# Optimization experiments

Hardware: AMD Instinct MI355X
Metric: run time of the kernel (lower is better)

Reference implementation:

```python
import jax, jax.numpy as jnp
import numpy as np

GROUPS = 8
N_HEADS = 8
EPS = 1e-5


def setup_inputs() -> dict:
    key = jax.random.key(0)
    ks = jax.random.split(key, 3)
    B, C, H, W = 8, 512, 32, 32
    x = jax.random.normal(ks[0], (B, C, H, W), dtype=jnp.float32)
    # Conv2d(C, 3C, 1) weight squeezed to [3C, C]; kaiming-ish scale
    qkv_w = jax.random.normal(ks[1], (3 * C, C), dtype=jnp.float32) * (1.0 / np.sqrt(C))
    proj_w = jax.random.normal(ks[2], (C, C), dtype=jnp.float32) * (1.0 / np.sqrt(C))
    return {
        "x": x,
        "norm_gamma": jnp.ones((C,), jnp.float32),
        "norm_beta": jnp.zeros((C,), jnp.float32),
        "qkv_w": qkv_w,
        "qkv_b": jnp.zeros((3 * C,), jnp.float32),
        "proj_w": proj_w,
        "proj_b": jnp.zeros((C,), jnp.float32),
    }


def reference(x, norm_gamma, norm_beta, qkv_w, qkv_b, proj_w, proj_b):
    B, C, H, W = x.shape
    nh = N_HEADS
    hd = C // nh
    scale = hd ** (-0.5)
    S = H * W

    # GroupNorm(8, C): normalize over (C/G, H, W) within each group
    xg = x.reshape(B, GROUPS, -1)
    mean = xg.mean(axis=-1, keepdims=True)
    var = xg.var(axis=-1, keepdims=True)
    xn = ((xg - mean) * jax.lax.rsqrt(var + EPS)).reshape(B, C, H, W)
    xn = xn * norm_gamma[None, :, None, None] + norm_beta[None, :, None, None]

    # 1x1 conv QKV == per-pixel matmul
    qkv = jnp.einsum('oc,bchw->bohw', qkv_w, xn) + qkv_b[None, :, None, None]
    qkv = qkv.reshape(B, 3, nh, hd, S)
    q, k, v = qkv[:, 0], qkv[:, 1], qkv[:, 2]  # each (B, nh, hd, S)

    # attn[b,h,s,t] = sum_d q[b,h,d,s] k[b,h,d,t] * scale
    attn = jax.nn.softmax(jnp.einsum('bhds,bhdt->bhst', q, k) * scale, axis=-1)
    out = jnp.einsum('bhst,bhdt->bhds', attn, v).reshape(B, C, H, W)

    # 1x1 conv projection + residual
    return x + jnp.einsum('oc,bchw->bohw', proj_w, out) + proj_b[None, :, None, None]
```

## Files before the change

### kernel.cpp

```cpp
#include <hip/hip_runtime.h>
#include <hip/hip_bf16.h>

typedef __attribute__((ext_vector_type(4))) float  f32x4;
typedef __attribute__((ext_vector_type(8))) _Float16 f16x8;
typedef __attribute__((ext_vector_type(4))) _Float16 f16x4;
typedef __attribute__((ext_vector_type(4))) float  float4v;
typedef __attribute__((ext_vector_type(4))) unsigned int uint4v;

#define BATCH   8
#define CDIM    512
#define SLEN    1024
#define NHEADS  8
#define HDIM    64
#define QSCALE  0.1803368801111f
#define FIXED_M 8.0f


__device__ __forceinline__ f32x4 mfma16x16x16f16(f16x4 a, f16x4 b, f32x4 c){
#if __has_builtin(__builtin_amdgcn_mfma_f32_16x16x16f16)
    return __builtin_amdgcn_mfma_f32_16x16x16f16(a, b, c, 0, 0, 0);
#else
    asm volatile("v_mfma_f32_16x16x16_f16 %0, %1, %2, %0"
                 : "+v"(c) : "v"(a), "v"(b));
    return c;
#endif
}

__device__ __forceinline__ float fast_exp2(float x){
    float r;
    asm("v_exp_f32 %0, %1" : "=v"(r) : "v"(x));
    return r;
}

__device__ __forceinline__ void stage16(const void* g, void* l, int lane){
#if __has_builtin(__builtin_amdgcn_global_load_lds)
    __builtin_amdgcn_global_load_lds((const __attribute__((address_space(1))) void*)g,
                                     (__attribute__((address_space(3))) void*)l, 16, 0, 0);
#else
    *(f16x8*)((char*)l + lane * 16) = *(const f16x8*)g;
#endif
}


__global__ __launch_bounds__(256) void prep(
    const float4v* __restrict__ qkvw, f16x4* __restrict__ wq,
    const float4v* __restrict__ projw, f16x4* __restrict__ pw,
    const float* __restrict__ x, float* __restrict__ part)
{
    __shared__ float s1[256], s2[256];
    if (blockIdx.x < 1024){
        int i = blockIdx.x * 256 + threadIdx.x;
        if (i < 196608){
            float4v v = qkvw[i];
            wq[i] = (f16x4){ (_Float16)v[0], (_Float16)v[1], (_Float16)v[2], (_Float16)v[3] };
        } else {
            int j = i - 196608;
            float4v v = projw[j];
            pw[j] = (f16x4){ (_Float16)v[0], (_Float16)v[1], (_Float16)v[2], (_Float16)v[3] };
        }
        return;
    }
    int bid = blockIdx.x - 1024;
    int bg = bid >> 3, pc = bid & 7;
    const float4v* xp = (const float4v*)(x + (size_t)bg * 65536 + (size_t)pc * 8192);
    float sum = 0.f, sq = 0.f;
    for (int i = threadIdx.x; i < 2048; i += 256){
        float4v v = xp[i];
        sum += (v[0] + v[1]) + (v[2] + v[3]);
        sq  += (v[0]*v[0] + v[1]*v[1]) + (v[2]*v[2] + v[3]*v[3]);
    }
    s1[threadIdx.x] = sum; s2[threadIdx.x] = sq;
    __syncthreads();
    for (int o = 128; o > 0; o >>= 1){
        if (threadIdx.x < o){ s1[threadIdx.x] += s1[threadIdx.x + o];
                              s2[threadIdx.x] += s2[threadIdx.x + o]; }
        __syncthreads();
    }
    if (threadIdx.x == 0){
        part[bid * 2 + 0] = s1[0];
        part[bid * 2 + 1] = s2[0];
    }
}


__global__ __launch_bounds__(256) void gn_apply(
    const float* __restrict__ x, const float* __restrict__ part,
    const float* __restrict__ gamma, const float* __restrict__ beta,
    _Float16* __restrict__ xnT)
{
    int b = blockIdx.z, g = blockIdx.y, s0 = blockIdx.x * 64;
    int bg = b * 8 + g, c0 = g * 64;

    float sum = 0.f, sq = 0.f;
#pragma unroll
    for (int p = 0; p < 8; p++){
        sum += part[bg * 16 + p * 2 + 0];
        sq  += part[bg * 16 + p * 2 + 1];
    }
    float mean = sum * (1.f / 65536.f);
    float var  = sq  * (1.f / 65536.f) - mean * mean;
    float inv  = rsqrtf(var + 1e-5f);

    __shared__ _Float16 tile[64 * 66];

    int tx = threadIdx.x & 15, ty = threadIdx.x >> 4;
#pragma unroll
    for (int j = 0; j < 4; j++){
        int c = ty + 16 * j;
        float ga = gamma[c0 + c] * inv;
        float be = beta[c0 + c] - mean * ga;
        float4v v = *(const float4v*)(x + ((size_t)(b * CDIM + c0 + c)) * SLEN + s0 + tx * 4);
#pragma unroll
        for (int i = 0; i < 4; i++)
            tile[(tx * 4 + i) * 66 + c] = (_Float16)(v[i] * ga + be);
    }
    __syncthreads();

    int s = threadIdx.x >> 2, cq = (threadIdx.x & 3) * 16;
    const unsigned int* lsrc = (const unsigned int*)((const unsigned short*)tile + s * 66 + cq);
    uint4v lo = { lsrc[0], lsrc[1], lsrc[2], lsrc[3] };
    uint4v hi = { lsrc[4], lsrc[5], lsrc[6], lsrc[7] };
    unsigned int* dst = (unsigned int*)(xnT + ((size_t)b * SLEN + s0 + s) * CDIM + c0 + cq);
    *(uint4v*)dst       = lo;
    *(uint4v*)(dst + 4) = hi;
}


#define GEMM_CORE(APTR, BPTR)                                                   \
    __shared__ __align__(16) char smem[34816];                                  \
    int tid = threadIdx.x;                                                      \
    int wid = tid >> 6, lane = tid & 63;                                        \
    int w0 = wid >> 1, w1 = wid & 1;                                            \
    int lr = lane & 15, lg = lane >> 4;                                         \
    int slotg = ((lane & 3) ^ ((lane >> 3) & 3)) * 16;                          \
    int srow = lane >> 2;                                                       \
    const char* agp = (const char*)(APTR) +                                     \
        ((size_t)(bo + wid * 32 + srow) * CDIM) * 2 + slotg;                    \
    const char* bgp = (const char*)(BPTR) +                                     \
        ((size_t)(sgbase + wid * 32 + srow) * CDIM) * 2 + slotg;                \
    char* lA = smem + wid * 2048;                                               \
    char* lB = smem + 8192 + wid * 2048;                                        \
    f32x4 acc[4][4];                                                            \
    _Pragma("unroll") for (int i = 0; i < 4; i++)                               \
    _Pragma("unroll") for (int j = 0; j < 4; j++)                               \
        acc[i][j] = (f32x4){0.f, 0.f, 0.f, 0.f};                                \
    _Pragma("unroll") for (int j = 0; j < 2; j++){                              \
        stage16(agp + j * 16384, lA + j * 1024, lane);                          \
        stage16(bgp + j * 16384, lB + j * 1024, lane);                          \
    }                                                                           \
    __syncthreads();                                                            \
    int xt = ((lr >> 1) & 3) << 4;                                              \
    for (int it = 0; it < 16; ++it){                                            \
        int cur = (it & 1) * 16384;                                             \
        if (it + 1 < 16){                                                       \
            int nxt = 16384 - cur, ko = (it + 1) * 64;                          \
            _Pragma("unroll") for (int j = 0; j < 2; j++){                      \
                stage16(agp + j * 16384 + ko, lA + nxt + j * 1024, lane);       \
                stage16(bgp + j * 16384 + ko, lB + nxt + j * 1024, lane);       \
            }                                                                   \
        }                                                                       \
        const char* Ac = smem + cur + (w0 * 64 + lr) * 64;                      \
        const char* Bc = smem + cur + 8192 + (w1 * 64 + lr) * 64;               \
        f16x8 af[4], bfr[4];                                                    \
        _Pragma("unroll") for (int t = 0; t < 4; t++){                          \
            af[t]  = *(const f16x8*)(Ac + t * 1024 + ((lg * 16) ^ xt));         \
            bfr[t] = *(const f16x8*)(Bc + t * 1024 + ((lg * 16) ^ xt));         \
        }                                                                       \
        _Pragma("unroll") for (int i = 0; i < 4; i++)                           \
        _Pragma("unroll") for (int j = 0; j < 4; j++)                           \
            acc[i][j] = __builtin_amdgcn_mfma_f32_16x16x32_f16(af[i], bfr[j],   \
                                                               acc[i][j], 0, 0, 0); \
        __syncthreads();                                                        \
    }


__global__ __launch_bounds__(256) void qkv_gemm(
    const _Float16* __restrict__ wq, const _Float16* __restrict__ xnT,
    const float* __restrict__ qkvb,
    _Float16* __restrict__ qT, _Float16* __restrict__ kT, _Float16* __restrict__ vv)
{
    int b  = blockIdx.z;
    int bo = blockIdx.y * 128;
    size_t sgbase = (size_t)b * SLEN + blockIdx.x * 128;

    GEMM_CORE(wq, xnT)

    int obase = bo + w0 * 64, sbase = blockIdx.x * 128 + w1 * 64;
    int p = obase >> 9;
    int h = (obase >> 6) & 7;
    size_t bh = (size_t)b * NHEADS + h;

    if (p == 2){
#pragma unroll
        for (int i = 0; i < 4; i++){
            int d0 = i * 16 + lg * 4;
            float4v bias = *(const float4v*)(qkvb + obase + d0);
#pragma unroll
            for (int j = 0; j < 4; j++){
                int s = sbase + j * 16 + lr;
                _Float16* vp2 = vv + (bh * HDIM) * SLEN + s;
                vp2[(size_t)(d0 + 0) * SLEN] = (_Float16)(acc[i][j][0] + bias[0]);
                vp2[(size_t)(d0 + 1) * SLEN] = (_Float16)(acc[i][j][1] + bias[1]);
                vp2[(size_t)(d0 + 2) * SLEN] = (_Float16)(acc[i][j][2] + bias[2]);
                vp2[(size_t)(d0 + 3) * SLEN] = (_Float16)(acc[i][j][3] + bias[3]);
            }
        }
    } else {
        float sc = (p == 0) ? QSCALE : 1.f;
        char* wreg = smem + wid * 8192;
#pragma unroll
        for (int i = 0; i < 4; i++){
            int d0 = i * 16 + lg * 4;
            float4v bias = *(const float4v*)(qkvb + obase + d0);
            int slotbase = (2 * i + (lg >> 1)) * 16;
            int inoff = (lg & 1) * 8;
#pragma unroll
            for (int j = 0; j < 4; j++){
                int s_loc = j * 16 + lr;
                f16x4 pk = { (_Float16)((acc[i][j][0] + bias[0]) * sc),
                             (_Float16)((acc[i][j][1] + bias[1]) * sc),
                             (_Float16)((acc[i][j][2] + bias[2]) * sc),
                             (_Float16)((acc[i][j][3] + bias[3]) * sc) };
                *(f16x4*)(wreg + s_loc * 128 + (slotbase ^ ((s_loc & 7) << 4)) + inoff) = pk;
            }
        }
        _Float16* dst = (p == 0 ? qT : kT) + (bh * SLEN + sbase) * HDIM;
#pragma unroll
        for (int m = 0; m < 8; m++){
            int s_loc = m * 8 + (lane >> 3);
            f16x8 row = *(const f16x8*)(wreg + s_loc * 128 + (((lane & 7) ^ (s_loc & 7)) << 4));
            *(f16x8*)(dst + (size_t)s_loc * HDIM + (lane & 7) * 8) = row;
        }
    }
}


__global__ __launch_bounds__(256) void proj_gemm(
    const _Float16* __restrict__ pw, const _Float16* __restrict__ outT,
    const float* __restrict__ pb, const float* __restrict__ x,
    float* __restrict__ y)
{
    int b  = blockIdx.z;
    int bo = blockIdx.y * 128;
    size_t sgbase = (size_t)b * SLEN + blockIdx.x * 128;

    GEMM_CORE(pw, outT)

    int obase = bo + w0 * 64, sbase = blockIdx.x * 128 + w1 * 64;
    float* wreg = (float*)(smem + wid * 8704);

#pragma unroll
    for (int half = 0; half < 2; half++){
        asm volatile("" ::: "memory");
#pragma unroll
        for (int jj = 0; jj < 2; jj++){
            int j = half * 2 + jj;
            int srow2 = jj * 16 + lr;
#pragma unroll
            for (int i = 0; i < 4; i++){
                int c0 = i * 16 + lg * 4;
                float4v bias = *(const float4v*)(pb + obase + c0);
                float4v v = { acc[i][j][0] + bias[0], acc[i][j][1] + bias[1],
                              acc[i][j][2] + bias[2], acc[i][j][3] + bias[3] };
                *(float4v*)(wreg + srow2 * 68 + c0) = v;
            }
        }
        asm volatile("" ::: "memory");
        int cl = lane >> 3, sq = (lane & 7) * 4;
#pragma unroll
        for (int g = 0; g < 8; g++){
            int c = cl + 8 * g;
            float r0 = wreg[(sq + 0) * 68 + c];
            float r1 = wreg[(sq + 1) * 68 + c];
            float r2 = wreg[(sq + 2) * 68 + c];
            float r3 = wreg[(sq + 3) * 68 + c];
            size_t idx = ((size_t)b * CDIM + obase + c) * SLEN + sbase + half * 32 + sq;
            float4v xr = *(const float4v*)(x + idx);
            float4v o = { r0 + xr[0], r1 + xr[1], r2 + xr[2], r3 + xr[3] };
            *(float4v*)(y + idx) = o;
        }
    }
}


#define ATTN_CHUNK(c)                                                           \
    {                                                                           \
        const char* kbuf = smem + ((c) & 3) * 16384;                            \
        const char* vbuf = kbuf + 8192;                                         \
        f16x8 kf[4][2];                                                         \
        _Pragma("unroll") for (int i = 0; i < 4; i++){                          \
            const char* kr = kbuf + (16 * i + lr) * 128;                        \
            kf[i][0] = *(const f16x8*)(kr + ((lg * 16) ^ r7));                  \
            kf[i][1] = *(const f16x8*)(kr + ((64 + lg * 16) ^ r7));             \
        }                                                                       \
        f16x4 vf[4][4];                                                         \
        _Pragma("unroll") for (int i = 0; i < 4; i++)                           \
        _Pragma("unroll") for (int dt = 0; dt < 4; dt++)                        \
            vf[i][dt] = *(const f16x4*)(vbuf + (dt * 16 + lr) * 128             \
                                        + ((32 * i + 8 * lg) ^ r7));            \
        _Pragma("unroll") for (int sj = 0; sj < 2; sj++){                       \
            f32x4 st[4];                                                        \
            _Pragma("unroll") for (int i = 0; i < 4; i++){                      \
                f32x4 z = (f32x4){-FIXED_M, -FIXED_M, -FIXED_M, -FIXED_M};      \
                z = __builtin_amdgcn_mfma_f32_16x16x32_f16(kf[i][0], qf[sj][0], z, 0, 0, 0); \
                z = __builtin_amdgcn_mfma_f32_16x16x32_f16(kf[i][1], qf[sj][1], z, 0, 0, 0); \
                st[i] = z;                                                      \
            }                                                                   \
            f16x4 pb[4];                                                        \
            _Pragma("unroll") for (int i = 0; i < 4; i++){                      \
                float p0 = fast_exp2(st[i][0]);                                 \
                float p1 = fast_exp2(st[i][1]);                                 \
                float p2 = fast_exp2(st[i][2]);                                 \
                float p3 = fast_exp2(st[i][3]);                                 \
                pb[i] = (f16x4){ (_Float16)p0, (_Float16)p1,                    \
                                 (_Float16)p2, (_Float16)p3 };                  \
            }                                                                   \
            _Pragma("unroll") for (int i = 0; i < 4; i++)                       \
                osum[sj] = mfma16x16x16f16(ones, pb[i], osum[sj]);              \
            _Pragma("unroll") for (int dt = 0; dt < 4; dt++){                   \
                f32x4 o = oac[dt][sj];                                          \
                _Pragma("unroll") for (int i = 0; i < 4; i++)                   \
                    o = mfma16x16x16f16(vf[i][dt], pb[i], o);                   \
                oac[dt][sj] = o;                                                \
            }                                                                   \
        }                                                                       \
    }

__global__ __launch_bounds__(256) void attn_kernel(
    const _Float16* __restrict__ qT, const _Float16* __restrict__ kT,
    const _Float16* __restrict__ vv, _Float16* __restrict__ outT)
{
    __shared__ __align__(16) char smem[65536];

    int id = blockIdx.x;
    int h = id & 7, rr = id >> 3;
    int sx = rr & 7, b = rr >> 3;
    size_t bh = (size_t)b * NHEADS + h;
    int tid = threadIdx.x;
    int wid = tid >> 6, lane = tid & 63;
    int lr = lane & 15, lg = lane >> 4;
    int sbase = sx * 128 + wid * 32;
    int phase = sx << 1;

    const _Float16* qp = qT + bh * SLEN * HDIM;
    const _Float16* kp = kT + bh * SLEN * HDIM;
    const _Float16* vp = vv + bh * HDIM * SLEN;

    int r8 = lane >> 3;
    int srow = wid * 16 + r8;
    int scol = ((lane & 7) * 16) ^ ((srow & 7) << 4);
    const char* kg = (const char*)kp + (size_t)srow * 128  + scol;
    const char* vg = (const char*)vp + (size_t)srow * 2048 + scol;
    char* kd = smem + wid * 2048;
    char* vd = smem + 8192 + wid * 2048;

    f16x8 qf[2][2];
#pragma unroll
    for (int sj = 0; sj < 2; sj++)
#pragma unroll
        for (int kk = 0; kk < 2; kk++)
            qf[sj][kk] = *(const f16x8*)(qp + (size_t)(sbase + sj * 16 + lr) * HDIM + kk * 32 + lg * 8);

    f32x4 oac[4][2], osum[2];
#pragma unroll
    for (int dt = 0; dt < 4; dt++){
        oac[dt][0] = (f32x4){0.f, 0.f, 0.f, 0.f};
        oac[dt][1] = (f32x4){0.f, 0.f, 0.f, 0.f};
    }
    osum[0] = (f32x4){0.f, 0.f, 0.f, 0.f};
    osum[1] = (f32x4){0.f, 0.f, 0.f, 0.f};
    const f16x4 ones = { (_Float16)1.f, (_Float16)1.f, (_Float16)1.f, (_Float16)1.f };

#pragma unroll
    for (int c = 0; c < 2; c++){
        int pc = (c + phase) & 15;
        stage16(kg + (size_t)pc * 8192,         kd + c * 16384,        lane);
        stage16(kg + (size_t)pc * 8192 + 1024,  kd + c * 16384 + 1024, lane);
        stage16(vg + (size_t)pc * 128,          vd + c * 16384,        lane);
        stage16(vg + (size_t)pc * 128 + 16384,  vd + c * 16384 + 1024, lane);
    }
    __syncthreads();

    int r7 = (lr & 7) << 4;

    for (int cc0 = 0; cc0 < 16; cc0 += 2){
        if (cc0 + 2 < 16){
#pragma unroll
            for (int u = 2; u < 4; u++){
                int lc = cc0 + u, pc = (lc + phase) & 15, bb = (lc & 3) * 16384;
                stage16(kg + (size_t)pc * 8192,         kd + bb,        lane);
                stage16(kg + (size_t)pc * 8192 + 1024,  kd + bb + 1024, lane);
                stage16(vg + (size_t)pc * 128,          vd + bb,        lane);
                stage16(vg + (size_t)pc * 128 + 16384,  vd + bb + 1024, lane);
            }
        }
        ATTN_CHUNK(cc0)
        ATTN_CHUNK(cc0 + 1)
        __syncthreads();
    }

#pragma unroll
    for (int sj = 0; sj < 2; sj++){
        float inv = 1.f / osum[sj][0];
        int s = sbase + sj * 16 + lr;
#pragma unroll
        for (int dt = 0; dt < 4; dt++){
            f16x4 ob = { (_Float16)(oac[dt][sj][0] * inv), (_Float16)(oac[dt][sj][1] * inv),
                         (_Float16)(oac[dt][sj][2] * inv), (_Float16)(oac[dt][sj][3] * inv) };
            *(f16x4*)(outT + ((size_t)b * SLEN + s) * CDIM + h * HDIM + dt * 16 + lg * 4) = ob;
        }
    }
}


extern "C" void kernel_launch(void* const* d_in, const int* in_sizes, int n_in,
                              void* d_out, int out_size, void* d_ws, size_t ws_size,
                              hipStream_t stream)
{
    const float* x     = (const float*)d_in[0];
    const float* gamma = (const float*)d_in[1];
    const float* beta  = (const float*)d_in[2];
    const float* qkvw  = (const float*)d_in[3];
    const float* qkvb  = (const float*)d_in[4];
    const float* projw = (const float*)d_in[5];
    const float* projb = (const float*)d_in[6];
    float* out = (float*)d_out;

    char* ws = (char*)d_ws;
    _Float16* wq_bf = (_Float16*)(ws);
    _Float16* pw_bf = (_Float16*)(ws + 1572864);
    _Float16* xnT   = (_Float16*)(ws + 2097152);
    _Float16* qT    = (_Float16*)(ws + 2097152 + 8388608);
    _Float16* kT    = (_Float16*)(ws + 2097152 + 16777216);
    _Float16* vv    = (_Float16*)(ws + 2097152 + 25165824);
    _Float16* outT  = (_Float16*)(ws + 2097152 + 33554432);
    float*    part  = (float*)(ws + 2097152 + 33554432);

    prep<<<1536, 256, 0, stream>>>((const float4v*)qkvw, (f16x4*)wq_bf,
                                   (const float4v*)projw, (f16x4*)pw_bf, x, part);
    gn_apply<<<dim3(16, 8, 8), 256, 0, stream>>>(x, part, gamma, beta, xnT);
    qkv_gemm<<<dim3(8, 12, 8), 256, 0, stream>>>(wq_bf, xnT, qkvb, qT, kT, vv);
    attn_kernel<<<512, 256, 0, stream>>>(qT, kT, vv, outT);
    proj_gemm<<<dim3(8, 4, 8), 256, 0, stream>>>(pw_bf, outT, projb, x, out);
}
```

Before: 79.40 us.

## Use 16x16x32 MFMA for PV and rowsum by permuting staged K rows

Replaces the 16x16x16 f16 MFMAs in the P·V and row-sum accumulation with 16x16x32 MFMAs that consume pairs of P fragments concatenated into 8-wide vectors. K rows are loaded into shared memory in a permuted order (sigma32), so the score fragment layout lines up with the wider MFMA's K dimension. V fragments are read as 8-wide LDS loads. This halves the MFMA instruction count in the inner attention loop and reduces LDS read instructions, at the cost of more complex row mapping that must stay consistent between K and V.

```diff
diff --git a/kernel.cpp b/kernel.cpp
--- a/kernel.cpp
+++ b/kernel.cpp
@@ -16,16 +16,6 @@
 #define FIXED_M 8.0f
 
 
-__device__ __forceinline__ f32x4 mfma16x16x16f16(f16x4 a, f16x4 b, f32x4 c){
-#if __has_builtin(__builtin_amdgcn_mfma_f32_16x16x16f16)
-    return __builtin_amdgcn_mfma_f32_16x16x16f16(a, b, c, 0, 0, 0);
-#else
-    asm volatile("v_mfma_f32_16x16x16_f16 %0, %1, %2, %0"
-                 : "+v"(c) : "v"(a), "v"(b));
-    return c;
-#endif
-}
-
 __device__ __forceinline__ float fast_exp2(float x){
     float r;
     asm("v_exp_f32 %0, %1" : "=v"(r) : "v"(x));
@@ -39,6 +29,10 @@
 #else
     *(f16x8*)((char*)l + lane * 16) = *(const f16x8*)g;
 #endif
+}
+
+__device__ __forceinline__ int sigma32(int p){
+    return 8 * ((p >> 2) & 3) + 4 * ((p >> 4) & 1) + (p & 3);
 }
 
 
@@ -293,11 +287,11 @@
             kf[i][0] = *(const f16x8*)(kr + ((lg * 16) ^ r7));                  \
             kf[i][1] = *(const f16x8*)(kr + ((64 + lg * 16) ^ r7));             \
         }                                                                       \
-        f16x4 vf[4][4];                                                         \
-        _Pragma("unroll") for (int i = 0; i < 4; i++)                           \
+        f16x8 vf8[2][4];                                                        \
+        _Pragma("unroll") for (int ip = 0; ip < 2; ip++)                        \
         _Pragma("unroll") for (int dt = 0; dt < 4; dt++)                        \
-            vf[i][dt] = *(const f16x4*)(vbuf + (dt * 16 + lr) * 128             \
-                                        + ((32 * i + 8 * lg) ^ r7));            \
+            vf8[ip][dt] = *(const f16x8*)(vbuf + (dt * 16 + lr) * 128           \
+                                          + ((ip * 64 + lg * 16) ^ r7));        \
         _Pragma("unroll") for (int sj = 0; sj < 2; sj++){                       \
             f32x4 st[4];                                                        \
             _Pragma("unroll") for (int i = 0; i < 4; i++){                      \
@@ -315,12 +309,14 @@
                 pb[i] = (f16x4){ (_Float16)p0, (_Float16)p1,                    \
                                  (_Float16)p2, (_Float16)p3 };                  \
             }                                                                   \
-            _Pragma("unroll") for (int i = 0; i < 4; i++)                       \
-                osum[sj] = mfma16x16x16f16(ones, pb[i], osum[sj]);              \
+            f16x8 pb8_0 = __builtin_shufflevector(pb[0], pb[1], 0,1,2,3,4,5,6,7); \
+            f16x8 pb8_1 = __builtin_shufflevector(pb[2], pb[3], 0,1,2,3,4,5,6,7); \
+            osum[sj] = __builtin_amdgcn_mfma_f32_16x16x32_f16(ones8, pb8_0, osum[sj], 0, 0, 0); \
+            osum[sj] = __builtin_amdgcn_mfma_f32_16x16x32_f16(ones8, pb8_1, osum[sj], 0, 0, 0); \
             _Pragma("unroll") for (int dt = 0; dt < 4; dt++){                   \
                 f32x4 o = oac[dt][sj];                                          \
-                _Pragma("unroll") for (int i = 0; i < 4; i++)                   \
-                    o = mfma16x16x16f16(vf[i][dt], pb[i], o);                   \
+                o = __builtin_amdgcn_mfma_f32_16x16x32_f16(vf8[0][dt], pb8_0, o, 0, 0, 0); \
+                o = __builtin_amdgcn_mfma_f32_16x16x32_f16(vf8[1][dt], pb8_1, o, 0, 0, 0); \
                 oac[dt][sj] = o;                                                \
             }                                                                   \
         }                                                                       \
@@ -347,10 +343,13 @@
     const _Float16* vp = vv + bh * HDIM * SLEN;
 
     int r8 = lane >> 3;
-    int srow = wid * 16 + r8;
-    int scol = ((lane & 7) * 16) ^ ((srow & 7) << 4);
-    const char* kg = (const char*)kp + (size_t)srow * 128  + scol;
-    const char* vg = (const char*)vp + (size_t)srow * 2048 + scol;
+    int p0 = wid * 16 + r8;
+    int tr0 = 32 * (p0 >> 5) + sigma32(p0 & 31);
+    int tr1 = 32 * ((p0 + 8) >> 5) + sigma32((p0 + 8) & 31);
+    int scol = ((lane & 7) * 16) ^ ((p0 & 7) << 4);
+    const char* kg0 = (const char*)kp + (size_t)tr0 * 128 + scol;
+    const char* kg1 = (const char*)kp + (size_t)tr1 * 128 + scol;
+    const char* vg  = (const char*)vp + (size_t)p0 * 2048 + scol;
     char* kd = smem + wid * 2048;
     char* vd = smem + 8192 + wid * 2048;
 
@@ -369,15 +368,16 @@
     }
     osum[0] = (f32x4){0.f, 0.f, 0.f, 0.f};
     osum[1] = (f32x4){0.f, 0.f, 0.f, 0.f};
-    const f16x4 ones = { (_Float16)1.f, (_Float16)1.f, (_Float16)1.f, (_Float16)1.f };
+    const f16x8 ones8 = { (_Float16)1.f, (_Float16)1.f, (_Float16)1.f, (_Float16)1.f,
+                          (_Float16)1.f, (_Float16)1.f, (_Float16)1.f, (_Float16)1.f };
 
 #pragma unroll
     for (int c = 0; c < 2; c++){
         int pc = (c + phase) & 15;
-        stage16(kg + (size_t)pc * 8192,         kd + c * 16384,        lane);
-        stage16(kg + (size_t)pc * 8192 + 1024,  kd + c * 16384 + 1024, lane);
-        stage16(vg + (size_t)pc * 128,          vd + c * 16384,        lane);
-        stage16(vg + (size_t)pc * 128 + 16384,  vd + c * 16384 + 1024, lane);
+        stage16(kg0 + (size_t)pc * 8192, kd + c * 16384,        lane);
+        stage16(kg1 + (size_t)pc * 8192, kd + c * 16384 + 1024, lane);
+        stage16(vg  + (size_t)pc * 128,          vd + c * 16384,        lane);
+        stage16(vg  + (size_t)pc * 128 + 16384,  vd + c * 16384 + 1024, lane);
     }
     __syncthreads();
 
@@ -388,10 +388,10 @@
 #pragma unroll
             for (int u = 2; u < 4; u++){
                 int lc = cc0 + u, pc = (lc + phase) & 15, bb = (lc & 3) * 16384;
-                stage16(kg + (size_t)pc * 8192,         kd + bb,        lane);
-                stage16(kg + (size_t)pc * 8192 + 1024,  kd + bb + 1024, lane);
-                stage16(vg + (size_t)pc * 128,          vd + bb,        lane);
-                stage16(vg + (size_t)pc * 128 + 16384,  vd + bb + 1024, lane);
+                stage16(kg0 + (size_t)pc * 8192, kd + bb,        lane);
+                stage16(kg1 + (size_t)pc * 8192, kd + bb + 1024, lane);
+                stage16(vg  + (size_t)pc * 128,          vd + bb,        lane);
+                stage16(vg  + (size_t)pc * 128 + 16384,  vd + bb + 1024, lane);
             }
         }
         ATTN_CHUNK(cc0)
```

Measured after the change: 76.33 us. 1.04x faster.
